# Performance work log

Measured on AMD Instinct MI355X. Metric: run time of the kernel, lower is better.

## Reference

```python
import jax, jax.numpy as jnp
import numpy as np

SIGMA = 1.0  # Gaussian perturbation scale


def setup_inputs() -> dict:
    key = jax.random.key(0)
    k1, k2, k3 = jax.random.split(key, 3)
    S, B, D = 64, 128, 10000
    theta = jax.random.normal(k1, (B, D), dtype=jnp.float32)
    y = jax.random.uniform(k2, (B, D), dtype=jnp.float32)
    noise = jax.random.normal(k3, (S, B, D), dtype=jnp.float32)  # eta = theta + SIGMA*noise
    return {"theta": theta, "y": y, "noise": noise}


def reference(theta, y, noise):
    # eta = ptb.sample(theta, samples=S): [S, B, D]
    eta = theta[None, :, :] + SIGMA * noise
    # oracle.call vectorized over (S, B): softmax over feature dim
    pi = jax.nn.softmax(eta, axis=-1)  # [S, B, D]
    # loss(pi[i], y) -> per-example vector [B]: MSE mean over features
    losses = jnp.mean((pi - y[None, :, :]) ** 2, axis=-1)  # [S, B]
    # val = losses.mean(dim=(0, 1)) -> scalar
    val = jnp.mean(losses)
    return val
```

## Files before the change

### kernel.cpp

```cpp
#include <hip/hip_runtime.h>

#define S_DIM 64
#define B_DIM 128
#define D_DIM 10000
#define NV4   2500
#define BLOCK 512
#define KMAX  5
#define RPB   8
#define NBLK  (B_DIM * (S_DIM / RPB))
#define NROWS (S_DIM * B_DIM)
#define NWAVE (BLOCK / 64)

__global__ __launch_bounds__(BLOCK) void perturbed_loss_lds(
    const float* __restrict__ theta,
    const float* __restrict__ y,
    const float* __restrict__ noise,
    float4* __restrict__ partials,
    float*  __restrict__ y2arr)
{
    __shared__ float Tlds[D_DIM];
    __shared__ float Vlds[D_DIM];
    __shared__ float redS[2][NWAVE], redQ[2][NWAVE], redP[2][NWAVE];
    __shared__ float redY[NWAVE];

    const int blk  = blockIdx.x;
    const int b    = blk >> 3;
    const int s0   = (blk & 7) * RPB;
    const int tid  = threadIdx.x;
    const int lane = tid & 63;
    const int wave = tid >> 6;

    const float4* th4 = reinterpret_cast<const float4*>(theta + (size_t)b * D_DIM);
    const float4* y4  = reinterpret_cast<const float4*>(y     + (size_t)b * D_DIM);
    float4* T4 = reinterpret_cast<float4*>(Tlds);
    float4* V4 = reinterpret_cast<float4*>(Vlds);

    float y2 = 0.0f;
    for (int i = tid; i < NV4; i += BLOCK) {
        float4 t  = th4[i];
        float4 yy = y4[i];
        float4 T, V;
        T.x = __expf(t.x); T.y = __expf(t.y);
        T.z = __expf(t.z); T.w = __expf(t.w);
        V.x = T.x * yy.x;  V.y = T.y * yy.y;
        V.z = T.z * yy.z;  V.w = T.w * yy.w;
        T4[i] = T;  V4[i] = V;
        y2 = fmaf(yy.x, yy.x, y2); y2 = fmaf(yy.y, yy.y, y2);
        y2 = fmaf(yy.z, yy.z, y2); y2 = fmaf(yy.w, yy.w, y2);
    }
    #pragma unroll
    for (int o = 32; o > 0; o >>= 1) y2 += __shfl_down(y2, o, 64);
    if (lane == 0) redY[wave] = y2;
    __syncthreads();
    if (tid == 0 && (blk & 7) == 0) {
        float t = 0.0f;
        #pragma unroll
        for (int w = 0; w < NWAVE; ++w) t += redY[w];
        y2arr[b] = t;
    }

    #pragma unroll 1
    for (int r = 0; r < RPB; ++r) {
        const int row = (s0 + r) * B_DIM + b;
        const float4* nz4 = reinterpret_cast<const float4*>(
            noise + (size_t)row * D_DIM);
        float s = 0.0f, q = 0.0f, p = 0.0f;
        #pragma unroll
        for (int k = 0; k < KMAX; ++k) {
            const int i = tid + k * BLOCK;
            if (k < KMAX - 1 || i < NV4) {
                float4 n = nz4[i];
                float4 T = T4[i];
                float4 V = V4[i];
                float e0 = __expf(n.x), e1 = __expf(n.y);
                float e2 = __expf(n.z), e3 = __expf(n.w);
                float t0 = T.x * e0, t1 = T.y * e1;
                float t2 = T.z * e2, t3 = T.w * e3;
                s += (t0 + t1) + (t2 + t3);
                q = fmaf(t0, t0, q); q = fmaf(t1, t1, q);
                q = fmaf(t2, t2, q); q = fmaf(t3, t3, q);
                p = fmaf(V.x, e0, p); p = fmaf(V.y, e1, p);
                p = fmaf(V.z, e2, p); p = fmaf(V.w, e3, p);
            }
        }
        #pragma unroll
        for (int o = 32; o > 0; o >>= 1) {
            s += __shfl_down(s, o, 64);
            q += __shfl_down(q, o, 64);
            p += __shfl_down(p, o, 64);
        }
        const int bb = r & 1;
        if (lane == 0) { redS[bb][wave] = s; redQ[bb][wave] = q; redP[bb][wave] = p; }
        __syncthreads();
        if (tid == 0) {
            float St = 0.0f, Qt = 0.0f, Pt = 0.0f;
            #pragma unroll
            for (int w = 0; w < NWAVE; ++w) {
                St += redS[bb][w]; Qt += redQ[bb][w]; Pt += redP[bb][w];
            }
            partials[row] = make_float4(St, Qt, Pt, 0.0f);
        }
    }
}

__global__ __launch_bounds__(256) void reduce_partials(
    const float4* __restrict__ partials,
    const float*  __restrict__ y2arr,
    float* __restrict__ out)
{
    __shared__ double red[4];
    const int tid  = threadIdx.x;
    const int lane = tid & 63;
    const int wave = tid >> 6;

    double acc = 0.0;
    for (int i = tid; i < NROWS; i += 256) {
        float4 r = partials[i];
        double invS = 1.0 / (double)r.x;
        acc += ((double)r.y * invS - 2.0 * (double)r.z) * invS
             + (double)y2arr[i & (B_DIM - 1)];
    }
    #pragma unroll
    for (int o = 32; o > 0; o >>= 1) acc += __shfl_down(acc, o, 64);
    if (lane == 0) red[wave] = acc;
    __syncthreads();
    if (tid == 0) {
        double t = ((red[0] + red[1]) + (red[2] + red[3]));
        out[0] = (float)(t / ((double)S_DIM * (double)B_DIM * (double)D_DIM));
    }
}

extern "C" void kernel_launch(void* const* d_in, const int* in_sizes, int n_in,
                              void* d_out, int out_size, void* d_ws, size_t ws_size,
                              hipStream_t stream) {
    const float* theta = (const float*)d_in[0];
    const float* y     = (const float*)d_in[1];
    const float* noise = (const float*)d_in[2];
    float* out       = (float*)d_out;
    float4* partials = (float4*)d_ws;
    float*  y2arr    = (float*)((char*)d_ws + NROWS * sizeof(float4));

    perturbed_loss_lds<<<NBLK, BLOCK, 0, stream>>>(theta, y, noise,
                                                   partials, y2arr);
    reduce_partials<<<1, 256, 0, stream>>>(partials, y2arr, out);
}
```

Baseline: 81.30 us.

## Assign one noise row per wave instead of block-wide row loop

Each of the 8 waves in a block now processes its own noise row (s0+wave) end to end, accumulating over 39 full strided iterations plus a 4-lane tail. This removes the per-row __syncthreads and cross-wave LDS reduction, so waves can run independently without block barriers between rows. In exchange, each wave reads a single contiguous 40KB row with only 64 lanes. That may change memory-level parallelism and DRAM access locality, and the 4-lane tail leaves most of the wave idle.

```diff
diff --git a/kernel.cpp b/kernel.cpp
--- a/kernel.cpp
+++ b/kernel.cpp
@@ -5,13 +5,13 @@
 #define D_DIM 10000
 #define NV4   2500
 #define BLOCK 512
-#define KMAX  5
 #define RPB   8
 #define NBLK  (B_DIM * (S_DIM / RPB))
 #define NROWS (S_DIM * B_DIM)
 #define NWAVE (BLOCK / 64)
+#define FULLIT 39
 
-__global__ __launch_bounds__(BLOCK) void perturbed_loss_lds(
+__global__ __launch_bounds__(BLOCK) void perturbed_loss_waverow(
     const float* __restrict__ theta,
     const float* __restrict__ y,
     const float* __restrict__ noise,
@@ -20,7 +20,6 @@
 {
     __shared__ float Tlds[D_DIM];
     __shared__ float Vlds[D_DIM];
-    __shared__ float redS[2][NWAVE], redQ[2][NWAVE], redP[2][NWAVE];
     __shared__ float redY[NWAVE];
 
     const int blk  = blockIdx.x;
@@ -59,48 +58,48 @@
         y2arr[b] = t;
     }
 
-    #pragma unroll 1
-    for (int r = 0; r < RPB; ++r) {
-        const int row = (s0 + r) * B_DIM + b;
-        const float4* nz4 = reinterpret_cast<const float4*>(
-            noise + (size_t)row * D_DIM);
-        float s = 0.0f, q = 0.0f, p = 0.0f;
-        #pragma unroll
-        for (int k = 0; k < KMAX; ++k) {
-            const int i = tid + k * BLOCK;
-            if (k < KMAX - 1 || i < NV4) {
-                float4 n = nz4[i];
-                float4 T = T4[i];
-                float4 V = V4[i];
-                float e0 = __expf(n.x), e1 = __expf(n.y);
-                float e2 = __expf(n.z), e3 = __expf(n.w);
-                float t0 = T.x * e0, t1 = T.y * e1;
-                float t2 = T.z * e2, t3 = T.w * e3;
-                s += (t0 + t1) + (t2 + t3);
-                q = fmaf(t0, t0, q); q = fmaf(t1, t1, q);
-                q = fmaf(t2, t2, q); q = fmaf(t3, t3, q);
-                p = fmaf(V.x, e0, p); p = fmaf(V.y, e1, p);
-                p = fmaf(V.z, e2, p); p = fmaf(V.w, e3, p);
-            }
-        }
-        #pragma unroll
-        for (int o = 32; o > 0; o >>= 1) {
-            s += __shfl_down(s, o, 64);
-            q += __shfl_down(q, o, 64);
-            p += __shfl_down(p, o, 64);
-        }
-        const int bb = r & 1;
-        if (lane == 0) { redS[bb][wave] = s; redQ[bb][wave] = q; redP[bb][wave] = p; }
-        __syncthreads();
-        if (tid == 0) {
-            float St = 0.0f, Qt = 0.0f, Pt = 0.0f;
-            #pragma unroll
-            for (int w = 0; w < NWAVE; ++w) {
-                St += redS[bb][w]; Qt += redQ[bb][w]; Pt += redP[bb][w];
-            }
-            partials[row] = make_float4(St, Qt, Pt, 0.0f);
-        }
+    const int row = (s0 + wave) * B_DIM + b;
+    const float4* nz4 = reinterpret_cast<const float4*>(noise + (size_t)row * D_DIM);
+
+    float s = 0.0f, q = 0.0f, p = 0.0f;
+    int i = lane;
+    #pragma unroll 4
+    for (int it = 0; it < FULLIT; ++it, i += 64) {
+        float4 n = nz4[i];
+        float4 T = T4[i];
+        float4 V = V4[i];
+        float e0 = __expf(n.x), e1 = __expf(n.y);
+        float e2 = __expf(n.z), e3 = __expf(n.w);
+        float t0 = T.x * e0, t1 = T.y * e1;
+        float t2 = T.z * e2, t3 = T.w * e3;
+        s += (t0 + t1) + (t2 + t3);
+        q = fmaf(t0, t0, q); q = fmaf(t1, t1, q);
+        q = fmaf(t2, t2, q); q = fmaf(t3, t3, q);
+        p = fmaf(V.x, e0, p); p = fmaf(V.y, e1, p);
+        p = fmaf(V.z, e2, p); p = fmaf(V.w, e3, p);
     }
+    if (lane < 4) {
+        const int it = FULLIT * 64 + lane;
+        float4 n = nz4[it];
+        float4 T = T4[it];
+        float4 V = V4[it];
+        float e0 = __expf(n.x), e1 = __expf(n.y);
+        float e2 = __expf(n.z), e3 = __expf(n.w);
+        float t0 = T.x * e0, t1 = T.y * e1;
+        float t2 = T.z * e2, t3 = T.w * e3;
+        s += (t0 + t1) + (t2 + t3);
+        q = fmaf(t0, t0, q); q = fmaf(t1, t1, q);
+        q = fmaf(t2, t2, q); q = fmaf(t3, t3, q);
+        p = fmaf(V.x, e0, p); p = fmaf(V.y, e1, p);
+        p = fmaf(V.z, e2, p); p = fmaf(V.w, e3, p);
+    }
+    #pragma unroll
+    for (int o = 32; o > 0; o >>= 1) {
+        s += __shfl_down(s, o, 64);
+        q += __shfl_down(q, o, 64);
+        p += __shfl_down(p, o, 64);
+    }
+    if (lane == 0) partials[row] = make_float4(s, q, p, 0.0f);
 }
 
 __global__ __launch_bounds__(256) void reduce_partials(
@@ -140,7 +139,7 @@
     float4* partials = (float4*)d_ws;
     float*  y2arr    = (float*)((char*)d_ws + NROWS * sizeof(float4));
 
-    perturbed_loss_lds<<<NBLK, BLOCK, 0, stream>>>(theta, y, noise,
-                                                   partials, y2arr);
+    perturbed_loss_waverow<<<NBLK, BLOCK, 0, stream>>>(theta, y, noise,
+                                                       partials, y2arr);
     reduce_partials<<<1, 256, 0, stream>>>(partials, y2arr, out);
 }
```

New measurement: 80.92 us. No clear change (-0.5%).
